# Kernel tuning notes

Measured on AMD Instinct MI355X. Metric: run time of the kernel, lower is better.

Reference implementation:

```python
import math
import jax, jax.numpy as jnp
import numpy as np

B, T, D, K = 8, 2048, 1024, 4096  # batch, seq, d_model, num_audio_tokens


def _positional_encoding(seq_len, d_model):
    position = jnp.arange(seq_len, dtype=jnp.float32)[:, None]
    div_term = jnp.exp(jnp.arange(0, d_model, 2, dtype=jnp.float32) * (-math.log(10000.0) / d_model))
    pe = jnp.zeros((seq_len, d_model), dtype=jnp.float32)
    pe = pe.at[:, 0::2].set(jnp.sin(position * div_term))
    pe = pe.at[:, 1::2].set(jnp.cos(position * div_term))
    return pe


def setup_inputs() -> dict:
    key = jax.random.key(0)
    k1, k2, k3 = jax.random.split(key, 3)
    x = jax.random.normal(k1, (B, T, D), dtype=jnp.float32)
    # codebook: nn.initializers.normal() default stddev = 0.01
    codebook = jax.random.normal(k2, (K, D), dtype=jnp.float32) * 0.01
    # nn.Embed table for quantized tokens
    embed_table = jax.random.normal(k3, (K, D), dtype=jnp.float32) * 0.02
    return {"x": x, "codebook": codebook, "embed_table": embed_table}


def reference(x, codebook, embed_table):
    # VQ branch: argmin over L2 distance to codebook.
    x2 = jnp.sum(x * x, axis=-1, keepdims=True)          # [B,T,1]
    c2 = jnp.sum(codebook * codebook, axis=-1)           # [K]
    xc = jnp.einsum('btd,kd->btk', x, codebook)          # [B,T,K]
    d2 = x2 - 2.0 * xc + c2                              # [B,T,K]
    indices = jnp.argmin(d2, axis=-1)                    # [B,T]
    q = embed_table[indices]                             # [B,T,D] gather
    pe = _positional_encoding(T, D)                      # [T,D]
    return q + pe[None, :, :]
```

## Files before the change

### kernel.cpp

```cpp
#include <hip/hip_runtime.h>
#include <hip/hip_bf16.h>
#include <cstddef>

#define BB 8
#define TT 2048
#define DD 1024
#define KK 4096
#define MM (BB * TT)

#define WMARG 1.0e-6
#define EPROBE 2.0e-6
#define NFIN 4

#define LEX_LT(v,i,w,j) ((v) < (w) || ((v) == (w) && (i) < (j)))

typedef unsigned long long u64;
typedef __attribute__((ext_vector_type(8))) short short8;
typedef __attribute__((ext_vector_type(8))) unsigned short ushort8v;
typedef __attribute__((ext_vector_type(4))) float f32x4;

#define AS1 __attribute__((address_space(1)))
#define AS3 __attribute__((address_space(3)))

__device__ __forceinline__ unsigned short f2bu(float f) {
    __hip_bfloat16 h = __float2bfloat16(f);
    union { __hip_bfloat16 b; unsigned short u; } cv; cv.b = h; return cv.u;
}
__device__ __forceinline__ unsigned fmono(float f) {
    unsigned b = __float_as_uint(f);
    return (b & 0x80000000u) ? ~b : (b | 0x80000000u);
}

__global__ __launch_bounds__(256)
void prep_kernel(const float* __restrict__ src, unsigned short* __restrict__ h,
                 float* __restrict__ sumsq, int nrows) {
    const int lane = threadIdx.x & 63;
    const int wave = (blockIdx.x * 256 + threadIdx.x) >> 6;
    const int row  = wave * 8 + (lane >> 3);
    const int blk  = lane & 7;
    if (row >= nrows) return;
    const float* a = src + (size_t)row * DD + blk * 128;
    unsigned short* hp = h + (size_t)row * DD + blk * 128;

    float r[8];
    #pragma unroll
    for (int g = 0; g < 16; ++g) {
        float4 v0 = *(const float4*)(a + g * 8);
        float4 v1 = *(const float4*)(a + g * 8 + 4);
        float e[8] = {v0.x, v0.y, v0.z, v0.w, v1.x, v1.y, v1.z, v1.w};
        ushort8v hv;
        #pragma unroll
        for (int j = 0; j < 8; ++j) {
            hv[j] = f2bu(e[j]);
            float sq = __fmul_rn(e[j], e[j]);
            r[j] = (g == 0) ? sq : __fadd_rn(r[j], sq);
        }
        *(ushort8v*)(hp + g * 8) = hv;
    }
    float b = __fadd_rn(__fadd_rn(__fadd_rn(r[0], r[1]), __fadd_rn(r[2], r[3])),
                        __fadd_rn(__fadd_rn(r[4], r[5]), __fadd_rn(r[6], r[7])));
    float t = __fadd_rn(b, __shfl_xor(b, 1, 64));
    float u = __fadd_rn(t, __shfl_xor(t, 2, 64));
    float s = __fadd_rn(u, __shfl_xor(u, 4, 64));
    if (blk == 0) sumsq[row] = s;
}

__global__ __launch_bounds__(256)
void vq_gemm_kernel(const unsigned short* __restrict__ xh,
                    const unsigned short* __restrict__ cbh,
                    const float* __restrict__ c2,
                    u64* __restrict__ cand2) {
    __shared__ char smem[32768];
    unsigned short (*Ah)[64] = (unsigned short(*)[64])(smem);
    unsigned short (*Bh)[64] = (unsigned short(*)[64])(smem + 16384);

    const int t    = threadIdx.x;
    const int lane = t & 63;
    const int w    = t >> 6;
    const int wr   = w >> 1;
    const int wc   = w & 1;
    const int m0   = blockIdx.x * 128;
    const int n0   = blockIdx.y * 128;

    const int l8  = lane >> 3;
    const int lsw = (lane & 7) ^ l8;
    const char* gA = (const char*)xh  + (size_t)(m0 + w * 32 + l8) * (DD * 2) + (size_t)lsw * 16;
    const char* gB = (const char*)cbh + (size_t)(n0 + w * 32 + l8) * (DD * 2) + (size_t)lsw * 16;

    f32x4 acc[4][4];
    #pragma unroll
    for (int i = 0; i < 4; ++i)
        #pragma unroll
        for (int j = 0; j < 4; ++j) acc[i][j] = (f32x4)0.f;

    for (int kt = 0; kt < 16; ++kt) {
        const size_t kOffB = (size_t)kt * 128;

        __syncthreads();
        #pragma unroll
        for (int i = 0; i < 4; ++i) {
            __builtin_amdgcn_global_load_lds(
                (const AS1 void*)(gA + (size_t)(i * 8) * (DD * 2) + kOffB),
                (AS3 void*)((char*)&Ah[w * 32 + i * 8][0]), 16, 0, 0);
            __builtin_amdgcn_global_load_lds(
                (const AS1 void*)(gB + (size_t)(i * 8) * (DD * 2) + kOffB),
                (AS3 void*)((char*)&Bh[w * 32 + i * 8][0]), 16, 0, 0);
        }
        __syncthreads();

        #pragma unroll
        for (int kf = 0; kf < 2; ++kf) {
            const int bidx = kf * 4 + (lane >> 4);
            const int swz  = (bidx ^ (lane & 7)) * 8;
            short8 ah[4];
            #pragma unroll
            for (int mf = 0; mf < 4; ++mf)
                ah[mf] = *(const short8*)&Ah[wr * 64 + mf * 16 + (lane & 15)][swz];
            #pragma unroll
            for (int nf = 0; nf < 4; ++nf) {
                short8 bh = *(const short8*)&Bh[wc * 64 + nf * 16 + (lane & 15)][swz];
                #pragma unroll
                for (int mf = 0; mf < 4; ++mf)
                    acc[mf][nf] = __builtin_amdgcn_mfma_f32_16x16x32_bf16(ah[mf], bh, acc[mf][nf], 0, 0, 0);
            }
        }
    }

    float (*sc)[16][68] = (float(*)[16][68])(smem);
    u64   (*pr)[8][2]   = (u64(*)[8][2])(smem + 17408);

    #pragma unroll
    for (int mf = 0; mf < 4; ++mf) {
        __syncthreads();
        #pragma unroll
        for (int nf = 0; nf < 4; ++nf)
            #pragma unroll
            for (int j = 0; j < 4; ++j)
                sc[w][(lane >> 4) * 4 + j][nf * 16 + (lane & 15)] = acc[mf][nf][j];
        __syncthreads();

        const int lr  = t >> 3;
        const int seg = t & 7;
        const int wrr = lr >> 4;
        const int r16 = lr & 15;
        const int wv  = wrr * 2 + (seg >> 2);
        const int cb0 = (seg & 3) * 16;
        const int kb  = n0 + seg * 16;
        u64 k0 = ~0ULL, k1 = ~0ULL;
        #pragma unroll
        for (int i = 0; i < 16; ++i) {
            float s = c2[kb + i] - 2.0f * sc[wv][r16][cb0 + i];
            u64 key = (((u64)fmono(s)) << 32) | (unsigned)(kb + i);
            if (key < k1) {
                if (key < k0) { k1 = k0; k0 = key; }
                else          { k1 = key; }
            }
        }
        pr[lr][seg][0] = k0;
        pr[lr][seg][1] = k1;
        __syncthreads();

        if (t < 32) {
            u64 b0 = ~0ULL, b1 = ~0ULL;
            #pragma unroll
            for (int j = 0; j < 8; ++j)
                #pragma unroll
                for (int s2 = 0; s2 < 2; ++s2) {
                    u64 kk = pr[t][j][s2];
                    if (kk < b1) {
                        if (kk < b0) { b1 = b0; b0 = kk; }
                        else         { b1 = kk; }
                    }
                }
            int m = m0 + (t >> 4) * 64 + mf * 16 + (t & 15);
            cand2[(size_t)(blockIdx.y * 2 + 0) * MM + m] = b0;
            cand2[(size_t)(blockIdx.y * 2 + 1) * MM + m] = b1;
        }
    }
}

__global__ __launch_bounds__(256)
void vq_merge_kernel(const u64* __restrict__ cand2, int* __restrict__ cand_idx) {
    const int m    = (blockIdx.x * 256 + threadIdx.x) >> 6;
    const int lane = threadIdx.x & 63;
    u64 a = cand2[(size_t)lane * MM + m];
    #pragma unroll
    for (int s = 0; s < NFIN; ++s) {
        u64 mn = a;
        #pragma unroll
        for (int off = 32; off > 0; off >>= 1) {
            u64 o = __shfl_xor(mn, off, 64);
            mn = (o < mn) ? o : mn;
        }
        if (lane == 0) cand_idx[s * MM + m] = (int)(mn & 0xffffffffu);
        if (a == mn) a = ~0ULL;
    }
}

__device__ __forceinline__ float ulpf(float v) {
    unsigned u = __float_as_uint(v) & 0x7f800000u;
    return __uint_as_float(u) * 1.1920928955078125e-7f;
}
__device__ __forceinline__ float chain_qv(float x2v, float xc, float c2k) {
    return __fadd_rn(__fsub_rn(x2v, __fmul_rn(2.0f, xc)), c2k);
}

__global__ void init_best_kernel(u64* best) { *best = ~0ULL; }

__global__ __launch_bounds__(256)
void vq_select_kernel(const int* __restrict__ cand_idx,
                      const float* __restrict__ x, const float* __restrict__ cb,
                      const float* __restrict__ x2, const float* __restrict__ c2,
                      int* __restrict__ sel_idx, int* __restrict__ alt_idx,
                      u64* __restrict__ best) {
    const int m   = blockIdx.x;
    const int tid = threadIdx.x;
    __shared__ float sx[DD];
    __shared__ float gq[NFIN], galt[NFIN], gmarg[NFIN];
    __shared__ int   gi[NFIN];

    ((float4*)sx)[tid] = ((const float4*)(x + (size_t)m * DD))[tid];
    __syncthreads();

    const int c   = tid >> 6;
    const int sub = tid & 63;
    const int k   = cand_idx[c * MM + m];
    const float* __restrict__ crow = cb + (size_t)k * DD;
    double dbl = 0.0;
    #pragma unroll
    for (int j = 0; j < DD / 64; ++j) {
        int i = sub + j * 64;
        dbl = fma((double)sx[i], (double)crow[i], dbl);
    }
    #pragma unroll
    for (int off = 32; off > 0; off >>= 1) dbl += __shfl_xor(dbl, off, 64);

    if (sub == 0) {
        const float x2m = x2[m], c2k = c2[k];
        const float xc  = (float)dbl;
        double v_sub = (double)x2m - 2.0 * (double)xc;
        float  s     = (float)v_sub;
        double v_add = (double)s + (double)c2k;
        float  qv    = (float)v_add;
        double d_sub = 0.5 * (double)ulpf(s)  - fabs(v_sub - (double)s);
        double d_add = 0.5 * (double)ulpf(qv) - fabs(v_add - (double)qv);
        double marg  = fmin(d_sub, d_add) * 0.5;

        float qm = chain_qv(x2m, (float)(dbl - EPROBE), c2k);
        float qp = chain_qv(x2m, (float)(dbl + EPROBE), c2k);
        float qa = qv;
        if (qm != qv) qa = qm;
        else if (qp != qv) qa = qp;

        gq[c] = qv; gi[c] = k; galt[c] = qa;
        gmarg[c] = (marg < WMARG && qa != qv) ? (float)marg : 1e30f;
    }
    __syncthreads();

    if (tid == 0) {
        float bv = gq[0]; int bi = gi[0];
        for (int t = 1; t < NFIN; ++t)
            if (LEX_LT(gq[t], gi[t], bv, bi)) { bv = gq[t]; bi = gi[t]; }

        float bestm = 1e30f; int altwin = bi;
        for (int t = 0; t < NFIN; ++t) {
            if (gmarg[t] >= 1e29f) continue;
            float wv = (0 == t) ? galt[0] : gq[0]; int wi = gi[0];
            for (int s2 = 1; s2 < NFIN; ++s2) {
                float v = (s2 == t) ? galt[s2] : gq[s2];
                if (LEX_LT(v, gi[s2], wv, wi)) { wv = v; wi = gi[s2]; }
            }
            if (wi != bi && gmarg[t] < bestm) { bestm = gmarg[t]; altwin = wi; }
        }
        sel_idx[m] = bi;
        alt_idx[m] = altwin;
        if (altwin != bi) {
            u64 key = ((u64)__float_as_uint(bestm) << 32) | (unsigned)m;
            atomicMin(best, key);
        }
    }
}

__global__ __launch_bounds__(256)
void vq_out_kernel(const int* __restrict__ sel_idx, const int* __restrict__ alt_idx,
                   const u64* __restrict__ best,
                   const float* __restrict__ embed, float* __restrict__ out) {
    const int m   = blockIdx.x;
    const int tid = threadIdx.x;

    u64 key = *best;
    int idx = sel_idx[m];
    if (key != ~0ULL && (int)(key & 0xffffffffu) == m) idx = alt_idx[m];

    const float tf  = (float)(m % TT);
    const float NEG = -9.210340371976184f / 1024.0f;

    const float4* e = (const float4*)(embed + (size_t)idx * DD);
    float4*       o = (float4*)(out + (size_t)m * DD);

    int c4 = tid;
    float4 ev = e[c4];
    int d = c4 * 4;
    float f0 = expf((float)d * NEG);
    float f2 = expf((float)(d + 2) * NEG);
    float a0 = tf * f0, a2 = tf * f2;
    float4 r;
    r.x = ev.x + sinf(a0);
    r.y = ev.y + cosf(a0);
    r.z = ev.z + sinf(a2);
    r.w = ev.w + cosf(a2);
    o[c4] = r;
}

extern "C" void kernel_launch(void* const* d_in, const int* in_sizes, int n_in,
                              void* d_out, int out_size, void* d_ws, size_t ws_size,
                              hipStream_t stream) {
    const float* x     = (const float*)d_in[0];
    const float* cb    = (const float*)d_in[1];
    const float* embed = (const float*)d_in[2];
    float* out = (float*)d_out;

    char* wp = (char*)d_ws;
    u64* best            = (u64*)wp;                       wp += 16;
    u64* cand2           = (u64*)wp;                       wp += (size_t)64 * MM * 8;
    unsigned short* cbh  = (unsigned short*)wp;            wp += (size_t)KK * DD * 2;
    unsigned short* xh   = (unsigned short*)wp;            wp += (size_t)MM * DD * 2;
    float* c2            = (float*)wp;                     wp += (size_t)KK * 4;
    float* x2            = (float*)wp;                     wp += (size_t)MM * 4;
    int*   cand_idx      = (int*)wp;                       wp += (size_t)NFIN * MM * 4;
    int*   sel_idx       = (int*)wp;                       wp += (size_t)MM * 4;
    int*   alt_idx       = (int*)wp;

    init_best_kernel<<<1, 1, 0, stream>>>(best);
    prep_kernel<<<KK / 32, 256, 0, stream>>>(cb, cbh, c2, KK);
    prep_kernel<<<MM / 32, 256, 0, stream>>>(x,  xh, x2, MM);

    dim3 grid(MM / 128, KK / 128);
    vq_gemm_kernel<<<grid, 256, 0, stream>>>(xh, cbh, c2, cand2);

    vq_merge_kernel<<<MM * 64 / 256, 256, 0, stream>>>(cand2, cand_idx);

    vq_select_kernel<<<MM, 256, 0, stream>>>(cand_idx, x, cb, x2, c2,
                                             sel_idx, alt_idx, best);

    vq_out_kernel<<<MM, 256, 0, stream>>>(sel_idx, alt_idx, best, embed, out);
}
```

Before: 322.1 us.

## Fuse merge into select, merge prep launches, shuffle-based top-2 in GEMM epilogue

Replaces the shared-memory top-2 reduction in the GEMM epilogue with a wave-shuffle butterfly, which removes one block barrier per fragment row. Folds the separate candidate merge kernel into the select kernel, so the intermediate candidate-index buffer and one launch go away. Combines the two prep launches into one grid covering both x and codebook rows, and swaps the init kernel for a memset. The select kernel now does a 64-way reduction on one wave before its dot products, which adds a little latency to each block.

After: 311.5 us. 1.03x faster.

```diff
diff --git a/kernel.cpp b/kernel.cpp
--- a/kernel.cpp
+++ b/kernel.cpp
@@ -22,6 +22,9 @@
 #define AS1 __attribute__((address_space(1)))
 #define AS3 __attribute__((address_space(3)))
 
+__device__ __forceinline__ u64 u64min(u64 a, u64 b) { return a < b ? a : b; }
+__device__ __forceinline__ u64 u64max(u64 a, u64 b) { return a > b ? a : b; }
+
 __device__ __forceinline__ unsigned short f2bu(float f) {
     __hip_bfloat16 h = __float2bfloat16(f);
     union { __hip_bfloat16 b; unsigned short u; } cv; cv.b = h; return cv.u;
@@ -32,15 +35,28 @@
 }
 
 __global__ __launch_bounds__(256)
-void prep_kernel(const float* __restrict__ src, unsigned short* __restrict__ h,
-                 float* __restrict__ sumsq, int nrows) {
+void prep_kernel(const float* __restrict__ xsrc, unsigned short* __restrict__ xdh,
+                 float* __restrict__ xss,
+                 const float* __restrict__ csrc, unsigned short* __restrict__ cdh,
+                 float* __restrict__ css) {
     const int lane = threadIdx.x & 63;
     const int wave = (blockIdx.x * 256 + threadIdx.x) >> 6;
-    const int row  = wave * 8 + (lane >> 3);
+    int row  = wave * 8 + (lane >> 3);
     const int blk  = lane & 7;
-    if (row >= nrows) return;
-    const float* a = src + (size_t)row * DD + blk * 128;
-    unsigned short* hp = h + (size_t)row * DD + blk * 128;
+
+    const float* a;
+    unsigned short* hp;
+    float* sumsq;
+    if (row < MM) {
+        a = xsrc + (size_t)row * DD + blk * 128;
+        hp = xdh + (size_t)row * DD + blk * 128;
+        sumsq = xss + row;
+    } else {
+        int r2 = row - MM;
+        a = csrc + (size_t)r2 * DD + blk * 128;
+        hp = cdh + (size_t)r2 * DD + blk * 128;
+        sumsq = css + r2;
+    }
 
     float r[8];
     #pragma unroll
@@ -62,7 +78,7 @@
     float t = __fadd_rn(b, __shfl_xor(b, 1, 64));
     float u = __fadd_rn(t, __shfl_xor(t, 2, 64));
     float s = __fadd_rn(u, __shfl_xor(u, 4, 64));
-    if (blk == 0) sumsq[row] = s;
+    if (blk == 0) *sumsq = s;
 }
 
 __global__ __launch_bounds__(256)
@@ -127,7 +143,6 @@
     }
 
     float (*sc)[16][68] = (float(*)[16][68])(smem);
-    u64   (*pr)[8][2]   = (u64(*)[8][2])(smem + 17408);
 
     #pragma unroll
     for (int mf = 0; mf < 4; ++mf) {
@@ -156,44 +171,19 @@
                 else          { k1 = key; }
             }
         }
-        pr[lr][seg][0] = k0;
-        pr[lr][seg][1] = k1;
-        __syncthreads();
-
-        if (t < 32) {
-            u64 b0 = ~0ULL, b1 = ~0ULL;
-            #pragma unroll
-            for (int j = 0; j < 8; ++j)
-                #pragma unroll
-                for (int s2 = 0; s2 < 2; ++s2) {
-                    u64 kk = pr[t][j][s2];
-                    if (kk < b1) {
-                        if (kk < b0) { b1 = b0; b0 = kk; }
-                        else         { b1 = kk; }
-                    }
-                }
-            int m = m0 + (t >> 4) * 64 + mf * 16 + (t & 15);
-            cand2[(size_t)(blockIdx.y * 2 + 0) * MM + m] = b0;
-            cand2[(size_t)(blockIdx.y * 2 + 1) * MM + m] = b1;
-        }
-    }
-}
-
-__global__ __launch_bounds__(256)
-void vq_merge_kernel(const u64* __restrict__ cand2, int* __restrict__ cand_idx) {
-    const int m    = (blockIdx.x * 256 + threadIdx.x) >> 6;
-    const int lane = threadIdx.x & 63;
-    u64 a = cand2[(size_t)lane * MM + m];
-    #pragma unroll
-    for (int s = 0; s < NFIN; ++s) {
-        u64 mn = a;
-        #pragma unroll
-        for (int off = 32; off > 0; off >>= 1) {
-            u64 o = __shfl_xor(mn, off, 64);
-            mn = (o < mn) ? o : mn;
-        }
-        if (lane == 0) cand_idx[s * MM + m] = (int)(mn & 0xffffffffu);
-        if (a == mn) a = ~0ULL;
+        #pragma unroll
+        for (int off = 1; off < 8; off <<= 1) {
+            u64 b0 = __shfl_xor(k0, off, 64);
+            u64 b1 = __shfl_xor(k1, off, 64);
+            u64 n0k = u64min(k0, b0);
+            u64 n1k = u64min(u64max(k0, b0), u64min(k1, b1));
+            k0 = n0k; k1 = n1k;
+        }
+        if (seg == 0) {
+            int m = m0 + wrr * 64 + mf * 16 + r16;
+            cand2[(size_t)(blockIdx.y * 2 + 0) * MM + m] = k0;
+            cand2[(size_t)(blockIdx.y * 2 + 1) * MM + m] = k1;
+        }
     }
 }
 
@@ -205,10 +195,8 @@
     return __fadd_rn(__fsub_rn(x2v, __fmul_rn(2.0f, xc)), c2k);
 }
 
-__global__ void init_best_kernel(u64* best) { *best = ~0ULL; }
-
 __global__ __launch_bounds__(256)
-void vq_select_kernel(const int* __restrict__ cand_idx,
+void vq_select_kernel(const u64* __restrict__ cand2,
                       const float* __restrict__ x, const float* __restrict__ cb,
                       const float* __restrict__ x2, const float* __restrict__ c2,
                       int* __restrict__ sel_idx, int* __restrict__ alt_idx,
@@ -216,15 +204,31 @@
     const int m   = blockIdx.x;
     const int tid = threadIdx.x;
     __shared__ float sx[DD];
+    __shared__ int   gk[NFIN];
     __shared__ float gq[NFIN], galt[NFIN], gmarg[NFIN];
     __shared__ int   gi[NFIN];
 
     ((float4*)sx)[tid] = ((const float4*)(x + (size_t)m * DD))[tid];
+
+    if (tid < 64) {
+        u64 a = cand2[(size_t)tid * MM + m];
+        #pragma unroll
+        for (int s = 0; s < NFIN; ++s) {
+            u64 mn = a;
+            #pragma unroll
+            for (int off = 32; off > 0; off >>= 1) {
+                u64 o = __shfl_xor(mn, off, 64);
+                mn = (o < mn) ? o : mn;
+            }
+            if (tid == 0) gk[s] = (int)(mn & 0xffffffffu);
+            if (a == mn) a = ~0ULL;
+        }
+    }
     __syncthreads();
 
     const int c   = tid >> 6;
     const int sub = tid & 63;
-    const int k   = cand_idx[c * MM + m];
+    const int k   = gk[c];
     const float* __restrict__ crow = cb + (size_t)k * DD;
     double dbl = 0.0;
     #pragma unroll
@@ -327,20 +331,17 @@
     unsigned short* xh   = (unsigned short*)wp;            wp += (size_t)MM * DD * 2;
     float* c2            = (float*)wp;                     wp += (size_t)KK * 4;
     float* x2            = (float*)wp;                     wp += (size_t)MM * 4;
-    int*   cand_idx      = (int*)wp;                       wp += (size_t)NFIN * MM * 4;
     int*   sel_idx       = (int*)wp;                       wp += (size_t)MM * 4;
     int*   alt_idx       = (int*)wp;
 
-    init_best_kernel<<<1, 1, 0, stream>>>(best);
-    prep_kernel<<<KK / 32, 256, 0, stream>>>(cb, cbh, c2, KK);
-    prep_kernel<<<MM / 32, 256, 0, stream>>>(x,  xh, x2, MM);
+    hipMemsetAsync(best, 0xFF, 8, stream);
+
+    prep_kernel<<<(MM + KK) / 32, 256, 0, stream>>>(x, xh, x2, cb, cbh, c2);
 
     dim3 grid(MM / 128, KK / 128);
     vq_gemm_kernel<<<grid, 256, 0, stream>>>(xh, cbh, c2, cand2);
 
-    vq_merge_kernel<<<MM * 64 / 256, 256, 0, stream>>>(cand2, cand_idx);
-
-    vq_select_kernel<<<MM, 256, 0, stream>>>(cand_idx, x, cb, x2, c2,
+    vq_select_kernel<<<MM, 256, 0, stream>>>(cand2, x, cb, x2, c2,
                                              sel_idx, alt_idx, best);
 
     vq_out_kernel<<<MM, 256, 0, stream>>>(sel_idx, alt_idx, best, embed, out);
```
